# Kernel optimization log

Measured on AMD Instinct MI355X. Metric: run time of the kernel, lower is better.

Reference implementation:

```python
import jax, jax.numpy as jnp
import numpy as np

# Static config (matches init_kwargs)
B, T_IN, H, W, C_IN = 32, 12, 64, 64, 4
T_OUT, C_OUT = 12, 4
K, S = 8, 4            # unfold kernel and stride (stride = K // 2); H%K==0 -> padding 0
DEC_K = 25             # series decomposition moving-average window
O = T_OUT * C_OUT      # number of per-output locally-connected filters
NH = (H - K) // S + 1  # 15
NW = (W - K) // S + 1  # 15
L = NH * NW            # 225 patches


def setup_inputs() -> dict:
    key = jax.random.key(0)
    k1, k2, k3 = jax.random.split(key, 3)
    x = jax.random.normal(k1, (B, T_IN, H, W, C_IN), jnp.float32)
    # torch init: weights ~ randn, biases zeros; stacked over the O = C_out*T_out loop
    w_s = jax.random.normal(k2, (O, T_IN, C_IN, K, K), jnp.float32)
    w_t = jax.random.normal(k3, (O, T_IN, C_IN, K, K), jnp.float32)
    b_s = jnp.zeros((O, K, K), jnp.float32)
    b_t = jnp.zeros((O, K, K), jnp.float32)
    return {"x": x, "w_s": w_s, "b_s": b_s, "w_t": w_t, "b_t": b_t}


def _moving_avg(x):
    # x: (B, T, N). Replicate-pad time by (DEC_K-1)//2 on each side, mean over DEC_K window.
    p = (DEC_K - 1) // 2
    xp = jnp.concatenate([jnp.repeat(x[:, :1], p, axis=1), x,
                          jnp.repeat(x[:, -1:], p, axis=1)], axis=1)
    cs = jnp.concatenate([jnp.zeros_like(xp[:, :1]), jnp.cumsum(xp, axis=1)], axis=1)
    return (cs[:, DEC_K:] - cs[:, :-DEC_K]) / DEC_K  # (B, T, N)


def _patch_idx():
    ii = (jnp.arange(NH) * S)[:, None] + jnp.arange(K)  # (NH, K)
    jj = (jnp.arange(NW) * S)[:, None] + jnp.arange(K)  # (NW, K)
    return ii, jj


def _unfold(x):
    # x: (B, Cc, H, W) -> patches (B, L, Cc, K, K), L row-major over (NH, NW) as in nn.Unfold
    ii, jj = _patch_idx()
    p = x[:, :, ii]              # (B, Cc, NH, K, W)
    p = p[:, :, :, :, jj]        # (B, Cc, NH, K, NW, K)
    p = p.transpose(0, 2, 4, 1, 3, 5)  # (B, NH, NW, Cc, K, K)
    return p.reshape(x.shape[0], L, x.shape[1], K, K)


def _fold(p):
    # p: (B, Cc, L, K, K) -> (B, Cc, H, W), summing overlapping contributions (nn.Fold)
    Bb, Cc = p.shape[0], p.shape[1]
    p = p.reshape(Bb, Cc, NH, NW, K, K).transpose(0, 1, 2, 4, 3, 5)  # (B,Cc,NH,K,NW,K)
    ii, jj = _patch_idx()
    I = ii[:, :, None, None]     # (NH, K, 1, 1)
    J = jj[None, None, :, :]     # (1, 1, NW, K)
    out = jnp.zeros((Bb, Cc, H, W), p.dtype)
    return out.at[:, :, I, J].add(p)


def reference(x, w_s, b_s, w_t, b_t):
    # (B, T, H, W, C) -> (B, T, C*H*W), decompose along time
    xf = x.transpose(0, 1, 4, 2, 3).reshape(B, T_IN, -1)
    trend = _moving_avg(xf)
    res = xf - trend
    out = jnp.zeros((B, L, O, K, K), x.dtype)
    for comp, w, b in ((res, w_s, b_s), (trend, w_t, b_t)):
        xc = comp.reshape(B, T_IN * C_IN, H, W)
        patches = _unfold(xc).reshape(B, L, T_IN, C_IN, K, K)
        # locally-connected linear: per (i,j) position, contract over (T_in, C_in) into O outputs
        out = out + jnp.einsum('bltcij,otcij->bloij', patches, w) + b
    out = out.transpose(0, 2, 1, 3, 4)            # (B, O, L, K, K)
    out = _fold(out)                              # (B, O, H, W)
    out = out.reshape(B, T_OUT, C_OUT, H, W).transpose(0, 1, 3, 4, 2)
    return out                                    # (B, T_out, H, W, C_out)
```

## Files before the change

kernel.cpp:

```cpp
#include <hip/hip_runtime.h>


typedef _Float16 h2 __attribute__((ext_vector_type(2)));
typedef _Float16 f16x8 __attribute__((ext_vector_type(8)));
typedef float f32x4 __attribute__((ext_vector_type(4)));
union F4F16 { float4 f4; f16x8 h8; };

__global__ __launch_bounds__(64) void pack_frags(const float* __restrict__ w_s,
                                                 const float* __restrict__ b_s,
                                                 const float* __restrict__ w_t,
                                                 const float* __restrict__ b_t,
                                                 float4* __restrict__ PWF) {
    int blk = blockIdx.x;
    int cls = blk / 12;
    int to = blk % 12;
    int L = threadIdx.x;
    int m16 = L & 15, quad = L >> 4;
    int c = m16 >> 2, r = m16 & 3;
    int o = to * 4 + c;
    int rh = cls >> 2, rw = cls & 3;
    int s = (rh + 4 * (r >> 1)) * 8 + (rw + 4 * (r & 1));
    const float* Wsb = w_s + (size_t)o * 3072 + s;
    const float* Wtb = w_t + (size_t)o * 3072 + s;
#pragma unroll
    for (int ks = 0; ks < 2; ++ks) {
        F4F16 u;
#pragma unroll
        for (int j = 0; j < 8; ++j) {
            int k = ks * 32 + quad * 8 + j;
            float val;
            if (k < 48) {
                val = Wsb[k * 64];
            } else if (k < 56) {
                int c2 = k & 3;
                bool isW1 = (k & 4) != 0;
                float acc = 0.f;
                for (int t = 0; t < 12; ++t) {
                    float d = Wtb[(t * 4 + c2) * 64] - Wsb[(t * 4 + c2) * 64];
                    acc += isW1 ? (float)t * d : d;
                }
                val = acc;
            } else if (k == 56) {
                val = b_s[o * 64 + s] + b_t[o * 64 + s];
            } else {
                val = 0.f;
            }
            u.h8[j] = (_Float16)val;
        }
        PWF[((size_t)blk * 2 + ks) * 64 + L] = u.f4;
    }
}

__global__ __launch_bounds__(256, 2) void dlinear_mfma(const float* __restrict__ x,
                                                       const float4* __restrict__ PWF,
                                                       float* __restrict__ out) {
    __shared__ float4 As[256 * 9];
    __shared__ __align__(16) float Es[4][256];
    int tid = threadIdx.x;
    int wv = tid >> 6, L = tid & 63;
    int cls = blockIdx.x & 15;
    int bb = blockIdx.x >> 4;
    int rh = cls >> 2, rw = cls & 3;

    f16x8 wf[12][2];
#pragma unroll
    for (int to = 0; to < 12; ++to)
#pragma unroll
        for (int ks = 0; ks < 2; ++ks) {
            F4F16 u;
            u.f4 = PWF[((size_t)(cls * 12 + to) * 2 + ks) * 64 + L];
            wf[to][ks] = u.h8;
        }

    int hh = tid >> 4, wwp = tid & 15;
    int h = 4 * hh + rh, wcol0 = 4 * wwp + rw;
    const float4* xb = (const float4*)x + (size_t)bb * 12 * 4096 + h * 64 + wcol0;

    h2 X2[32] __attribute__((aligned(16)));
    {
        float sx = 0.f, sy = 0.f, sz = 0.f, sw = 0.f;
        float4 first, last;
#pragma unroll
        for (int t = 0; t < 12; ++t) {
            float4 v = xb[t * 4096];
            if (t == 0) first = v;
            if (t == 11) last = v;
            h2 a, b;
            a[0] = (_Float16)v.x; a[1] = (_Float16)v.y;
            b[0] = (_Float16)v.z; b[1] = (_Float16)v.w;
            X2[2 * t] = a;
            X2[2 * t + 1] = b;
            sx += v.x; sy += v.y; sz += v.z; sw += v.w;
        }
        const float inv25 = 1.f / 25.f;
        float A0 = (sx + 12.f * first.x + last.x) * inv25;
        float A1 = (sy + 12.f * first.y + last.y) * inv25;
        float A2 = (sz + 12.f * first.z + last.z) * inv25;
        float A3 = (sw + 12.f * first.w + last.w) * inv25;
        float D0 = (last.x - first.x) * inv25;
        float D1 = (last.y - first.y) * inv25;
        float D2 = (last.z - first.z) * inv25;
        float D3 = (last.w - first.w) * inv25;
        h2 t0, t1, t2, t3, t4, z;
        t0[0] = (_Float16)A0; t0[1] = (_Float16)A1;
        t1[0] = (_Float16)A2; t1[1] = (_Float16)A3;
        t2[0] = (_Float16)D0; t2[1] = (_Float16)D1;
        t3[0] = (_Float16)D2; t3[1] = (_Float16)D3;
        t4[0] = (_Float16)1.f; t4[1] = (_Float16)0.f;
        z[0] = (_Float16)0.f; z[1] = (_Float16)0.f;
        X2[24] = t0; X2[25] = t1; X2[26] = t2; X2[27] = t3;
        X2[28] = t4; X2[29] = z; X2[30] = z; X2[31] = z;
    }
#pragma unroll
    for (int j = 0; j < 8; ++j) As[tid * 9 + j] = ((float4*)X2)[j];
    __syncthreads();

    int quad = L >> 4, nlane = L & 15;
    f16x8 pf[4][2];
#pragma unroll
    for (int g = 0; g < 4; ++g) {
        int p = wv * 64 + g * 16 + nlane;
#pragma unroll
        for (int ks = 0; ks < 2; ++ks) {
            F4F16 u;
            u.f4 = As[p * 9 + ks * 4 + quad];
            pf[g][ks] = u.h8;
        }
    }

    bool okw0 = nlane <= 14, okw1 = nlane >= 1;
    float4* ob = (float4*)out + (size_t)bb * 12 * 4096;
    int rdpix = wv * 64 + L;
    int st_hh = rdpix >> 4, st_ww = rdpix & 15;
    float4* stp = ob + (4 * st_hh + rh) * 64 + (4 * st_ww + rw);

#pragma unroll
    for (int to = 0; to < 12; ++to) {
#pragma unroll
        for (int g = 0; g < 4; ++g) {
            f32x4 d = {0.f, 0.f, 0.f, 0.f};
            d = __builtin_amdgcn_mfma_f32_16x16x32_f16(wf[to][0], pf[g][0], d, 0, 0, 0);
            d = __builtin_amdgcn_mfma_f32_16x16x32_f16(wf[to][1], pf[g][1], d, 0, 0, 0);
            int hq = wv * 4 + g;
            bool okh0 = hq <= 14, okh1 = hq >= 1;
            float v = ((okh0 && okw0) ? d[0] : 0.f)
                    + ((okh0 && okw1) ? d[1] : 0.f)
                    + ((okh1 && okw0) ? d[2] : 0.f)
                    + ((okh1 && okw1) ? d[3] : 0.f);
            Es[wv][g * 64 + nlane * 4 + quad] = v;
        }
        float4 r = *(const float4*)&Es[wv][4 * L];
        stp[to * 4096] = r;
    }
}

extern "C" void kernel_launch(void* const* d_in, const int* in_sizes, int n_in,
                              void* d_out, int out_size, void* d_ws, size_t ws_size,
                              hipStream_t stream) {
    const float* x = (const float*)d_in[0];
    const float* w_s = (const float*)d_in[1];
    const float* b_s = (const float*)d_in[2];
    const float* w_t = (const float*)d_in[3];
    const float* b_t = (const float*)d_in[4];
    float* out = (float*)d_out;
    float4* PWF = (float4*)d_ws;

    pack_frags<<<192, 64, 0, stream>>>(w_s, b_s, w_t, b_t, PWF);
    dlinear_mfma<<<32 * 16, 256, 0, stream>>>(x, PWF, out);
}
```

Measured before the change: 112.7 us.

## Restructure MFMA kernel for coalesced contiguous pixel loads and stores

Each block in the main kernel now covers one row-residue and half the image width across all four column residues, using 512 threads. Each thread loads contiguous pixels, so global reads and the output float4 writes are coalesced instead of strided by four. Weight fragments are loaded in two halves to cut register pressure, which costs per-timestep block-wide barriers through LDS. The weight-packing kernel is also parallelized across 256 threads, with the t-weighted reductions shared through LDS.

```diff
diff --git a/kernel.cpp b/kernel.cpp
--- a/kernel.cpp
+++ b/kernel.cpp
@@ -4,77 +4,82 @@
 typedef _Float16 h2 __attribute__((ext_vector_type(2)));
 typedef _Float16 f16x8 __attribute__((ext_vector_type(8)));
 typedef float f32x4 __attribute__((ext_vector_type(4)));
-union F4F16 { float4 f4; f16x8 h8; };
-
-__global__ __launch_bounds__(64) void pack_frags(const float* __restrict__ w_s,
-                                                 const float* __restrict__ b_s,
-                                                 const float* __restrict__ w_t,
-                                                 const float* __restrict__ b_t,
-                                                 float4* __restrict__ PWF) {
+union F2H8 { struct { float2 lo, hi; } f; f16x8 h8; };
+union HU { _Float16 h; unsigned short u; };
+
+__global__ __launch_bounds__(256) void pack_frags(const float* __restrict__ w_s,
+                                                  const float* __restrict__ b_s,
+                                                  const float* __restrict__ w_t,
+                                                  const float* __restrict__ b_t,
+                                                  uint2* __restrict__ PWF) {
+    __shared__ float W01[2][16][4];
     int blk = blockIdx.x;
-    int cls = blk / 12;
-    int to = blk % 12;
-    int L = threadIdx.x;
-    int m16 = L & 15, quad = L >> 4;
-    int c = m16 >> 2, r = m16 & 3;
+    int cls = blk / 12, to = blk % 12;
+    int rh = cls >> 2, rw = cls & 3;
+    int tid = threadIdx.x;
+
+    if (tid < 64) {
+        int m16 = tid >> 2, cin = tid & 3;
+        int c = m16 >> 2, rr = m16 & 3;
+        int o = to * 4 + c;
+        int s = (rh + 4 * (rr >> 1)) * 8 + (rw + 4 * (rr & 1));
+        float a0 = 0.f, a1 = 0.f;
+#pragma unroll
+        for (int t = 0; t < 12; ++t) {
+            int base = ((o * 12 + t) * 4 + cin) * 64 + s;
+            float d = w_t[base] - w_s[base];
+            a0 += d;
+            a1 += (float)t * d;
+        }
+        W01[0][m16][cin] = a0;
+        W01[1][m16][cin] = a1;
+    }
+    __syncthreads();
+
+    int ks = tid >> 7, jh = (tid >> 6) & 1, L = tid & 63;
+    int quad = L >> 4, m16 = L & 15;
+    int c = m16 >> 2, rr = m16 & 3;
     int o = to * 4 + c;
-    int rh = cls >> 2, rw = cls & 3;
-    int s = (rh + 4 * (r >> 1)) * 8 + (rw + 4 * (r & 1));
-    const float* Wsb = w_s + (size_t)o * 3072 + s;
-    const float* Wtb = w_t + (size_t)o * 3072 + s;
-#pragma unroll
-    for (int ks = 0; ks < 2; ++ks) {
-        F4F16 u;
-#pragma unroll
-        for (int j = 0; j < 8; ++j) {
-            int k = ks * 32 + quad * 8 + j;
-            float val;
-            if (k < 48) {
-                val = Wsb[k * 64];
-            } else if (k < 56) {
-                int c2 = k & 3;
-                bool isW1 = (k & 4) != 0;
-                float acc = 0.f;
-                for (int t = 0; t < 12; ++t) {
-                    float d = Wtb[(t * 4 + c2) * 64] - Wsb[(t * 4 + c2) * 64];
-                    acc += isW1 ? (float)t * d : d;
-                }
-                val = acc;
-            } else if (k == 56) {
-                val = b_s[o * 64 + s] + b_t[o * 64 + s];
-            } else {
-                val = 0.f;
-            }
-            u.h8[j] = (_Float16)val;
-        }
-        PWF[((size_t)blk * 2 + ks) * 64 + L] = u.f4;
-    }
+    int s = (rh + 4 * (rr >> 1)) * 8 + (rw + 4 * (rr & 1));
+    unsigned short us[4];
+#pragma unroll
+    for (int j4 = 0; j4 < 4; ++j4) {
+        int j = jh * 4 + j4;
+        int k = ks * 32 + quad * 8 + j;
+        float val;
+        if (k < 48) {
+            val = w_s[((o * 12 + (k >> 2)) * 4 + (k & 3)) * 64 + s];
+        } else if (k < 56) {
+            val = W01[(k >> 2) & 1][m16][k & 3];
+        } else if (k == 56) {
+            val = b_s[o * 64 + s] + b_t[o * 64 + s];
+        } else {
+            val = 0.f;
+        }
+        HU hu;
+        hu.h = (_Float16)val;
+        us[j4] = hu.u;
+    }
+    uint2 pk;
+    pk.x = (unsigned)us[0] | ((unsigned)us[1] << 16);
+    pk.y = (unsigned)us[2] | ((unsigned)us[3] << 16);
+    PWF[((size_t)(blk * 2 + ks) * 64 + L) * 2 + jh] = pk;
 }
 
-__global__ __launch_bounds__(256, 2) void dlinear_mfma(const float* __restrict__ x,
+__global__ __launch_bounds__(512, 4) void dlinear_mfma(const float* __restrict__ x,
                                                        const float4* __restrict__ PWF,
                                                        float* __restrict__ out) {
-    __shared__ float4 As[256 * 9];
-    __shared__ __align__(16) float Es[4][256];
+    __shared__ __align__(16) float2 As2[512 * 17];
+    __shared__ float Es[512 * 5];
     int tid = threadIdx.x;
     int wv = tid >> 6, L = tid & 63;
-    int cls = blockIdx.x & 15;
-    int bb = blockIdx.x >> 4;
-    int rh = cls >> 2, rw = cls & 3;
-
-    f16x8 wf[12][2];
-#pragma unroll
-    for (int to = 0; to < 12; ++to)
-#pragma unroll
-        for (int ks = 0; ks < 2; ++ks) {
-            F4F16 u;
-            u.f4 = PWF[((size_t)(cls * 12 + to) * 2 + ks) * 64 + L];
-            wf[to][ks] = u.h8;
-        }
-
-    int hh = tid >> 4, wwp = tid & 15;
-    int h = 4 * hh + rh, wcol0 = 4 * wwp + rw;
-    const float4* xb = (const float4*)x + (size_t)bb * 12 * 4096 + h * 64 + wcol0;
+    unsigned bx = blockIdx.x;
+    int wh = bx & 1, rh = (bx >> 1) & 3;
+    int bb = bx >> 3;
+
+    int a = tid >> 5, cw = tid & 31;
+    int h = 4 * a + rh, wimg = wh * 32 + cw;
+    const float4* xb = (const float4*)x + (size_t)bb * 12 * 4096 + h * 64 + wimg;
 
     h2 X2[32] __attribute__((aligned(16)));
     {
@@ -85,11 +90,11 @@
             float4 v = xb[t * 4096];
             if (t == 0) first = v;
             if (t == 11) last = v;
-            h2 a, b;
-            a[0] = (_Float16)v.x; a[1] = (_Float16)v.y;
-            b[0] = (_Float16)v.z; b[1] = (_Float16)v.w;
-            X2[2 * t] = a;
-            X2[2 * t + 1] = b;
+            h2 aa, bbh;
+            aa[0] = (_Float16)v.x; aa[1] = (_Float16)v.y;
+            bbh[0] = (_Float16)v.z; bbh[1] = (_Float16)v.w;
+            X2[2 * t] = aa;
+            X2[2 * t + 1] = bbh;
             sx += v.x; sy += v.y; sz += v.z; sw += v.w;
         }
         const float inv25 = 1.f / 25.f;
@@ -111,46 +116,78 @@
         X2[24] = t0; X2[25] = t1; X2[26] = t2; X2[27] = t3;
         X2[28] = t4; X2[29] = z; X2[30] = z; X2[31] = z;
     }
-#pragma unroll
-    for (int j = 0; j < 8; ++j) As[tid * 9 + j] = ((float4*)X2)[j];
+    {
+        const float2* xf2 = (const float2*)X2;
+#pragma unroll
+        for (int j = 0; j < 16; ++j) As2[17 * tid + j] = xf2[j];
+    }
     __syncthreads();
 
     int quad = L >> 4, nlane = L & 15;
+    int rcls = wv & 3, ghalf = wv >> 2;
+    int cls = rh * 4 + rcls;
     f16x8 pf[4][2];
 #pragma unroll
     for (int g = 0; g < 4; ++g) {
-        int p = wv * 64 + g * 16 + nlane;
+        int G = ghalf * 4 + g;
+        int p = 64 * G + 32 * (nlane >> 3) + 4 * (nlane & 7) + rcls;
+        int base = 17 * p;
 #pragma unroll
         for (int ks = 0; ks < 2; ++ks) {
-            F4F16 u;
-            u.f4 = As[p * 9 + ks * 4 + quad];
+            F2H8 u;
+            u.f.lo = As2[base + ks * 8 + quad * 2];
+            u.f.hi = As2[base + ks * 8 + quad * 2 + 1];
             pf[g][ks] = u.h8;
         }
     }
 
-    bool okw0 = nlane <= 14, okw1 = nlane >= 1;
+    int rp = nlane >> 3, ci = nlane & 7;
+    int wwp = wh * 8 + ci;
+    bool okw0 = wwp <= 14, okw1 = wwp >= 1;
+
     float4* ob = (float4*)out + (size_t)bb * 12 * 4096;
-    int rdpix = wv * 64 + L;
-    int st_hh = rdpix >> 4, st_ww = rdpix & 15;
-    float4* stp = ob + (4 * st_hh + rh) * 64 + (4 * st_ww + rw);
-
-#pragma unroll
-    for (int to = 0; to < 12; ++to) {
-#pragma unroll
-        for (int g = 0; g < 4; ++g) {
-            f32x4 d = {0.f, 0.f, 0.f, 0.f};
-            d = __builtin_amdgcn_mfma_f32_16x16x32_f16(wf[to][0], pf[g][0], d, 0, 0, 0);
-            d = __builtin_amdgcn_mfma_f32_16x16x32_f16(wf[to][1], pf[g][1], d, 0, 0, 0);
-            int hq = wv * 4 + g;
-            bool okh0 = hq <= 14, okh1 = hq >= 1;
-            float v = ((okh0 && okw0) ? d[0] : 0.f)
-                    + ((okh0 && okw1) ? d[1] : 0.f)
-                    + ((okh1 && okw0) ? d[2] : 0.f)
-                    + ((okh1 && okw1) ? d[3] : 0.f);
-            Es[wv][g * 64 + nlane * 4 + quad] = v;
-        }
-        float4 r = *(const float4*)&Es[wv][4 * L];
-        stp[to * 4096] = r;
+    float4* stp = ob + h * 64 + wimg;
+
+#pragma unroll 1
+    for (int toh = 0; toh < 2; ++toh) {
+        f16x8 wf[6][2];
+#pragma unroll
+        for (int tt = 0; tt < 6; ++tt)
+#pragma unroll
+            for (int ks = 0; ks < 2; ++ks) {
+                F2H8 u;
+                const float4 v = PWF[((size_t)(cls * 12 + toh * 6 + tt) * 2 + ks) * 64 + L];
+                u.f.lo = make_float2(v.x, v.y);
+                u.f.hi = make_float2(v.z, v.w);
+                wf[tt][ks] = u.h8;
+            }
+#pragma unroll 1
+        for (int tt = 0; tt < 6; ++tt) {
+            int to = toh * 6 + tt;
+#pragma unroll
+            for (int g = 0; g < 4; ++g) {
+                int G = ghalf * 4 + g;
+                f32x4 d = {0.f, 0.f, 0.f, 0.f};
+                d = __builtin_amdgcn_mfma_f32_16x16x32_f16(wf[tt][0], pf[g][0], d, 0, 0, 0);
+                d = __builtin_amdgcn_mfma_f32_16x16x32_f16(wf[tt][1], pf[g][1], d, 0, 0, 0);
+                int hhl = 2 * G + rp;
+                bool okh0 = hhl <= 14, okh1 = hhl >= 1;
+                float v = ((okh0 && okw0) ? d[0] : 0.f)
+                        + ((okh0 && okw1) ? d[1] : 0.f)
+                        + ((okh1 && okw0) ? d[2] : 0.f)
+                        + ((okh1 && okw1) ? d[3] : 0.f);
+                int p = 64 * G + 32 * rp + 4 * ci + rcls;
+                Es[5 * p + quad] = v;
+            }
+            __syncthreads();
+            float4 r;
+            r.x = Es[5 * tid + 0];
+            r.y = Es[5 * tid + 1];
+            r.z = Es[5 * tid + 2];
+            r.w = Es[5 * tid + 3];
+            stp[to * 4096] = r;
+            __syncthreads();
+        }
     }
 }
 
@@ -163,8 +200,8 @@
     const float* w_t = (const float*)d_in[3];
     const float* b_t = (const float*)d_in[4];
     float* out = (float*)d_out;
-    float4* PWF = (float4*)d_ws;
-
-    pack_frags<<<192, 64, 0, stream>>>(w_s, b_s, w_t, b_t, PWF);
-    dlinear_mfma<<<32 * 16, 256, 0, stream>>>(x, PWF, out);
+    void* PWF = d_ws;
+
+    pack_frags<<<192, 256, 0, stream>>>(w_s, b_s, w_t, b_t, (uint2*)PWF);
+    dlinear_mfma<<<32 * 4 * 2, 512, 0, stream>>>(x, (const float4*)PWF, out);
 }
```

Result: faster. 107.3 us (-4.7%).
